# Performance work log

Measured on AMD Instinct MI355X. Metric: run time of the kernel, lower is better.

Reference implementation:

```python
import jax, jax.numpy as jnp
import numpy as np

N_NODES = 100000
N_EDGES = 1600000
IN_CH = 48
OUT_CH = 64
K = 2


def setup_inputs() -> dict:
    key = jax.random.key(0)
    k1, k2, k3, k4 = jax.random.split(key, 4)
    x = jax.random.normal(k1, (N_NODES, IN_CH), dtype=jnp.float32)
    edge_index = jax.random.randint(k2, (2, N_EDGES), 0, N_NODES, dtype=jnp.int64)
    W = jax.random.normal(k3, (IN_CH, OUT_CH), dtype=jnp.float32) * (1.0 / np.sqrt(IN_CH))
    b = jax.random.normal(k4, (OUT_CH,), dtype=jnp.float32) * 0.01
    return {"x": x, "edge_index": edge_index, "W": W, "b": b}


def _propagate(x, row, col):
    n = x.shape[0]
    # degree of each node counted over col (destination) indices
    deg = jax.ops.segment_sum(jnp.ones_like(col, dtype=x.dtype), col, num_segments=n)
    deg_inv_sqrt = jnp.where(deg > 0, jax.lax.rsqrt(jnp.where(deg > 0, deg, 1.0)), 0.0)
    norm = deg_inv_sqrt[row] * deg_inv_sqrt[col]  # [E]
    # gather-scale-scatter: out[col] += x[row] * norm
    msgs = x[row] * norm[:, None]  # [E, d]
    return jax.ops.segment_sum(msgs, col, num_segments=n)


def reference(x, edge_index, W, b):
    row, col = edge_index[0], edge_index[1]
    h = x
    for _ in range(K):
        h = _propagate(h, row, col)
    return h @ W + b
```

## Files before the change

kernel.cpp:

```cpp
#include <hip/hip_runtime.h>
#include <hip/hip_bf16.h>
#include <hip/hip_fp16.h>


#define N_NODES 100000
#define N_EDGES 1600000
#define IN_CH 48
#define OUT_CH 64
#define NBUCKETS 392
#define CAP 4608
#define EPB 8192
#define NBLK_EDGE 196
#define NBLK_BKT 391

__global__ void init_kernel(int* __restrict__ bucketCursor, int* __restrict__ binTotal) {
    int t = threadIdx.x;
    if (t < NBUCKETS) bucketCursor[t] = t * CAP;
    if (t < 64) binTotal[t] = 0;
}

__global__ void bucket_scatter_kernel(const int* __restrict__ row, const int* __restrict__ col,
                                      int* __restrict__ bucketCursor, int* __restrict__ edge_packed) {
    __shared__ int lh[NBUCKETS];
    __shared__ int lofs[NBUCKETS];
    __shared__ int lbase[NBUCKETS];
    __shared__ int stage[EPB];
    __shared__ unsigned short sbkt[EPB];
    __shared__ int wsum[4];
    int tid = threadIdx.x;
    int base = blockIdx.x * EPB;
    for (int i = tid; i < NBUCKETS; i += 256) lh[i] = 0;
    __syncthreads();
    #pragma unroll 4
    for (int k = 0; k < 32; k++) {
        int e = base + k * 256 + tid;
        if (e < N_EDGES) atomicAdd(&lh[col[e] >> 8], 1);
    }
    __syncthreads();
    {
        int c0 = (tid < 196) ? lh[2 * tid] : 0;
        int c1 = (tid < 196) ? lh[2 * tid + 1] : 0;
        int s = c0 + c1;
        int incl = s;
        int lane = tid & 63, w = tid >> 6;
        #pragma unroll
        for (int o = 1; o < 64; o <<= 1) {
            int v = __shfl_up(incl, o, 64);
            if (lane >= o) incl += v;
        }
        if (lane == 63) wsum[w] = incl;
        __syncthreads();
        int wbase = 0;
        for (int k = 0; k < w; k++) wbase += wsum[k];
        int ex = wbase + incl - s;
        if (tid < 196) {
            lofs[2 * tid]     = ex;
            lofs[2 * tid + 1] = ex + c0;
        }
    }
    __syncthreads();
    for (int i = tid; i < NBUCKETS; i += 256) {
        int c = lh[i];
        if (c > 0) lbase[i] = atomicAdd(&bucketCursor[i], c);
        lh[i] = 0;
    }
    __syncthreads();
    #pragma unroll 4
    for (int k = 0; k < 32; k++) {
        int e = base + k * 256 + tid;
        if (e < N_EDGES) {
            int c = col[e];
            int bkt = c >> 8;
            int r = atomicAdd(&lh[bkt], 1);
            int slot = lofs[bkt] + r;
            stage[slot] = (row[e] << 8) | (c & 255);
            sbkt[slot] = (unsigned short)bkt;
        }
    }
    __syncthreads();
    int total = (base + EPB <= N_EDGES) ? EPB : (N_EDGES - base);
    for (int i = tid; i < total; i += 256) {
        int bkt = sbkt[i];
        int dst = lbase[bkt] + (i - lofs[bkt]);
        if (dst < (bkt + 1) * CAP)
            edge_packed[dst] = stage[i];
    }
}

__global__ void fine_sort_kernel(const int* __restrict__ edge_packed,
                                 const int* __restrict__ bucketCursor,
                                 const float* __restrict__ x,
                                 int* __restrict__ edge_src,
                                 int* __restrict__ deg, int* __restrict__ start,
                                 float* __restrict__ dis, int* __restrict__ binTotal,
                                 __half2* __restrict__ xs) {
    __shared__ int fh[256];
    __shared__ int cur[256];
    __shared__ int bh[64];
    __shared__ float fdis[256];
    __shared__ int wsum2[4];
    int b = blockIdx.x;
    int t = threadIdx.x;
    int s0 = b * CAP;
    int s1 = min(bucketCursor[b], (b + 1) * CAP);
    int nodeBase = b << 8;
    fh[t] = 0;
    if (t < 64) bh[t] = 0;
    __syncthreads();
    for (int j = s0 + t; j < s1; j += 256)
        atomicAdd(&fh[edge_packed[j] & 255], 1);
    __syncthreads();
    int c = fh[t];
    int incl = c;
    {
        int sl = t & 63, sw = t >> 6;
        #pragma unroll
        for (int o = 1; o < 64; o <<= 1) {
            int v = __shfl_up(incl, o, 64);
            if (sl >= o) incl += v;
        }
        if (sl == 63) wsum2[sw] = incl;
        __syncthreads();
        int wbase = 0;
        for (int k = 0; k < sw; k++) wbase += wsum2[k];
        incl += wbase;
    }
    int ex = incl - c;
    int node = nodeBase + t;
    bool valid = (node < N_NODES);
    int d = c;
    float dv = (valid && d > 0) ? rsqrtf((float)d) : 0.0f;
    cur[t] = ex;
    fdis[t] = dv;
    if (valid) {
        deg[node] = d;
        start[node] = s0 + ex;
        dis[node] = dv;
        atomicAdd(&bh[min(d, 63)], 1);
    }
    __syncthreads();
    for (int i = t; i < 256 * 24; i += 256) {
        int ln = i / 24;
        int nd = nodeBase + ln;
        if (nd < N_NODES) {
            int ci = i - ln * 24;
            float dd = fdis[ln];
            float2 v = ((const float2*)x)[nd * 24 + ci];
            xs[nd * 24 + ci] = __floats2half2_rn(v.x * dd, v.y * dd);
        }
    }
    for (int j = s0 + t; j < s1; j += 256) {
        int rc = edge_packed[j];
        int p = atomicAdd(&cur[rc & 255], 1);
        edge_src[s0 + p] = rc >> 8;
    }
    __syncthreads();
    if (t < 64 && bh[t]) atomicAdd(&binTotal[t], bh[t]);
}

__global__ void binscan_kernel(const int* __restrict__ binTotal, int* __restrict__ binCursor) {
    if (threadIdx.x == 0) {
        int s = 0;
        for (int k = 63; k >= 0; k--) { binCursor[k] = s; s += binTotal[k]; }
    }
}

__global__ void order_kernel(const int* __restrict__ deg, const int* __restrict__ start,
                             const float* __restrict__ dis, int* __restrict__ binCursor,
                             int4* __restrict__ nodeinfo, int n) {
    __shared__ int lhist[64];
    __shared__ int lbase[64];
    int i = blockIdx.x * 256 + threadIdx.x;
    if (threadIdx.x < 64) lhist[threadIdx.x] = 0;
    __syncthreads();
    int bin = 0, myrank = 0;
    if (i < n) {
        bin = min(deg[i], 63);
        myrank = atomicAdd(&lhist[bin], 1);
    }
    __syncthreads();
    if (threadIdx.x < 64 && lhist[threadIdx.x] > 0)
        lbase[threadIdx.x] = atomicAdd(&binCursor[threadIdx.x], lhist[threadIdx.x]);
    __syncthreads();
    if (i < n)
        nodeinfo[lbase[bin] + myrank] = make_int4(i, start[i], deg[i], __float_as_int(dis[i]));
}

#define LOAD3(p, v0, v1, v2) { v0 = (p)[0]; v1 = (p)[1]; v2 = (p)[2]; }
#define ACC6(v0, v1, v2) { \
    float2 u0 = __half22float2(v0), u1 = __half22float2(v1), u2 = __half22float2(v2); \
    a0 += u0.x; a1 += u0.y; a2 += u1.x; a3 += u1.y; a4 += u2.x; a5 += u2.y; }
#define ACC6B(v0, v1, v2) { \
    float2 u0 = __half22float2(v0), u1 = __half22float2(v1), u2 = __half22float2(v2); \
    b0 += u0.x; b1 += u0.y; b2 += u1.x; b3 += u1.y; b4 += u2.x; b5 += u2.y; }

#define DECLD(P) __half2 P##00,P##01,P##02,P##10,P##11,P##12,P##20,P##21,P##22,P##30,P##31,P##32
#define DECLS(S) int S##0, S##1, S##2, S##3
#define LOADSRC(S) { S##0 = edge_src[j]; S##1 = edge_src[j+1]; \
                     S##2 = edge_src[j+2]; S##3 = edge_src[j+3]; j += 4; }
#define ISSUED(P, S, basep) { \
    const __half2* q0 = basep + S##0 * 24 + lane3; \
    const __half2* q1 = basep + S##1 * 24 + lane3; \
    const __half2* q2 = basep + S##2 * 24 + lane3; \
    const __half2* q3 = basep + S##3 * 24 + lane3; \
    P##00 = q0[0]; P##01 = q0[1]; P##02 = q0[2]; \
    P##10 = q1[0]; P##11 = q1[1]; P##12 = q1[2]; \
    P##20 = q2[0]; P##21 = q2[1]; P##22 = q2[2]; \
    P##30 = q3[0]; P##31 = q3[1]; P##32 = q3[2]; }
#define CONSUMED(P) { ACC6(P##00,P##01,P##02); ACC6B(P##10,P##11,P##12); \
                      ACC6(P##20,P##21,P##22); ACC6B(P##30,P##31,P##32); }

#define GATHER_PIPELINE(basep) { \
    int m = (e - s) >> 2; \
    DECLD(A); DECLD(B); \
    DECLS(sa); DECLS(sb); \
    if (m >= 2) { \
        LOADSRC(sa); LOADSRC(sb); \
        ISSUED(A, sa, basep); \
        m -= 2; \
        while (m >= 2) { \
            LOADSRC(sa); \
            ISSUED(B, sb, basep); \
            CONSUMED(A); \
            LOADSRC(sb); \
            ISSUED(A, sa, basep); \
            CONSUMED(B); \
            m -= 2; \
        } \
        if (m == 1) { \
            LOADSRC(sa); \
            ISSUED(B, sb, basep); \
            CONSUMED(A); \
            ISSUED(A, sa, basep); \
            CONSUMED(B); \
            CONSUMED(A); \
        } else { \
            ISSUED(B, sb, basep); \
            CONSUMED(A); \
            CONSUMED(B); \
        } \
    } else if (m == 1) { \
        LOADSRC(sa); \
        ISSUED(A, sa, basep); \
        CONSUMED(A); \
    } \
    for (; j < e; ++j) { \
        const __half2* p0 = basep + edge_src[j] * 24 + lane3; \
        __half2 v00, v01, v02; \
        LOAD3(p0, v00, v01, v02); \
        ACC6(v00, v01, v02); \
    } \
    a0 += b0; a1 += b1; a2 += b2; a3 += b3; a4 += b4; a5 += b5; }

__global__ void gather1_kernel(const __half2* __restrict__ xs,
                               const int* __restrict__ edge_src,
                               const int4* __restrict__ nodeinfo,
                               __half2* __restrict__ h1) {
    int g = blockIdx.x * 32 + (threadIdx.x >> 3);
    int lane3 = (threadIdx.x & 7) * 3;
    int4 ni = nodeinfo[g];
    int node = ni.x, s = ni.y, e = s + ni.z;
    float dv = __int_as_float(ni.w);
    float a0 = 0, a1 = 0, a2 = 0, a3 = 0, a4 = 0, a5 = 0;
    float b0 = 0, b1 = 0, b2 = 0, b3 = 0, b4 = 0, b5 = 0;
    int j = s;
    GATHER_PIPELINE(xs);
    float sc = dv * dv;
    __half2* q = h1 + node * 24 + lane3;
    q[0] = __floats2half2_rn(a0 * sc, a1 * sc);
    q[1] = __floats2half2_rn(a2 * sc, a3 * sc);
    q[2] = __floats2half2_rn(a4 * sc, a5 * sc);
}

__global__ void gather2_gemm_kernel(const __half2* __restrict__ h1,
                                    const int* __restrict__ edge_src,
                                    const int4* __restrict__ nodeinfo,
                                    const float* __restrict__ W,
                                    const float* __restrict__ bias,
                                    float* __restrict__ out) {
    __shared__ float sW[IN_CH * OUT_CH];
    __shared__ float sb[OUT_CH];
    __shared__ float sh[32][IN_CH + 1];

    for (int i = threadIdx.x; i < IN_CH * OUT_CH; i += 256) sW[i] = W[i];
    if (threadIdx.x < OUT_CH) sb[threadIdx.x] = bias[threadIdx.x];

    int nl = threadIdx.x >> 3;
    int lane = threadIdx.x & 7;
    int lane3 = lane * 3;
    int g = blockIdx.x * 32 + nl;
    int4 ni = nodeinfo[g];
    int node = ni.x, s = ni.y, e = s + ni.z;
    float dv = __int_as_float(ni.w);

    float a0 = 0, a1 = 0, a2 = 0, a3 = 0, a4 = 0, a5 = 0;
    float b0 = 0, b1 = 0, b2 = 0, b3 = 0, b4 = 0, b5 = 0;
    int j = s;
    GATHER_PIPELINE(h1);
    int c0 = 6 * lane;
    sh[nl][c0 + 0] = a0 * dv;
    sh[nl][c0 + 1] = a1 * dv;
    sh[nl][c0 + 2] = a2 * dv;
    sh[nl][c0 + 3] = a3 * dv;
    sh[nl][c0 + 4] = a4 * dv;
    sh[nl][c0 + 5] = a5 * dv;
    __syncthreads();

    int j0 = lane * 8;
    float acc[8];
    #pragma unroll
    for (int i = 0; i < 8; i++) acc[i] = sb[j0 + i];
    for (int k = 0; k < IN_CH; k++) {
        float s0 = sh[nl][k];
        #pragma unroll
        for (int i = 0; i < 8; i++) acc[i] += s0 * sW[k * OUT_CH + j0 + i];
    }
    float4* o = (float4*)(out + (size_t)node * OUT_CH + j0);
    o[0] = make_float4(acc[0], acc[1], acc[2], acc[3]);
    o[1] = make_float4(acc[4], acc[5], acc[6], acc[7]);
}

extern "C" void kernel_launch(void* const* d_in, const int* in_sizes, int n_in,
                              void* d_out, int out_size, void* d_ws, size_t ws_size,
                              hipStream_t stream) {
    const float* x   = (const float*)d_in[0];
    const int*   ei  = (const int*)d_in[1];
    const float* W   = (const float*)d_in[2];
    const float* b   = (const float*)d_in[3];
    float* out = (float*)d_out;

    const int* row = ei;
    const int* col = ei + N_EDGES;

    int* ws_i = (int*)d_ws;
    int* bucketCursor = ws_i;
    int* binTotal     = ws_i + 512;
    int* binCursor    = ws_i + 576;
    int* deg          = ws_i + 1024;
    int* start        = ws_i + 101376;
    float* dis        = (float*)(ws_i + 201728);
    int4* nodeinfo    = (int4*)(ws_i + 302080);
    int* edge_packed  = ws_i + 703488;
    int* edge_src     = ws_i + 2509824;
    __half2* xs       = (__half2*)(ws_i + 4316160);
    __half2* h1       = (__half2*)(ws_i + 6716160);

    init_kernel<<<1, 512, 0, stream>>>(bucketCursor, binTotal);
    bucket_scatter_kernel<<<NBLK_EDGE, 256, 0, stream>>>(row, col, bucketCursor, edge_packed);
    fine_sort_kernel<<<NBLK_BKT, 256, 0, stream>>>(edge_packed, bucketCursor, x,
                                                   edge_src, deg, start, dis, binTotal, xs);
    binscan_kernel<<<1, 64, 0, stream>>>(binTotal, binCursor);
    order_kernel<<<(N_NODES + 255) / 256, 256, 0, stream>>>(deg, start, dis, binCursor,
                                                            nodeinfo, N_NODES);

    gather1_kernel<<<N_NODES / 32, 256, 0, stream>>>(xs, edge_src, nodeinfo, h1);
    gather2_gemm_kernel<<<N_NODES / 32, 256, 0, stream>>>(h1, edge_src, nodeinfo, W, b, out);
}
```

Measured before the change: 228.2 us.

## Pad gather rows to 128B, split scaling kernel, shrink edge-bucketing blocks

Node feature rows in xs and h1 are padded from 24 to 32 half2, so each 96-byte row starts on a 128-byte boundary and gathers touch fewer cache lines. The x-scaling-to-fp16 work moves out of fine_sort into its own fully parallel scale_kernel, and xs reuses the edge_packed workspace region. The edge bucketing kernel now handles 2048 edges per block instead of 8192, giving more and lighter blocks. The trade-offs are a 33% larger feature footprint, one extra kernel launch, and more global atomics on the bucket cursors.

```diff
diff --git a/kernel.cpp b/kernel.cpp
--- a/kernel.cpp
+++ b/kernel.cpp
@@ -9,9 +9,11 @@
 #define OUT_CH 64
 #define NBUCKETS 392
 #define CAP 4608
-#define EPB 8192
-#define NBLK_EDGE 196
+#define EPB 2048
+#define EPR 8
+#define NBLK_EDGE 782
 #define NBLK_BKT 391
+#define RSTRIDE 32
 
 __global__ void init_kernel(int* __restrict__ bucketCursor, int* __restrict__ binTotal) {
     int t = threadIdx.x;
@@ -31,8 +33,8 @@
     int base = blockIdx.x * EPB;
     for (int i = tid; i < NBUCKETS; i += 256) lh[i] = 0;
     __syncthreads();
-    #pragma unroll 4
-    for (int k = 0; k < 32; k++) {
+    #pragma unroll
+    for (int k = 0; k < EPR; k++) {
         int e = base + k * 256 + tid;
         if (e < N_EDGES) atomicAdd(&lh[col[e] >> 8], 1);
     }
@@ -65,8 +67,8 @@
         lh[i] = 0;
     }
     __syncthreads();
-    #pragma unroll 4
-    for (int k = 0; k < 32; k++) {
+    #pragma unroll
+    for (int k = 0; k < EPR; k++) {
         int e = base + k * 256 + tid;
         if (e < N_EDGES) {
             int c = col[e];
@@ -89,15 +91,12 @@
 
 __global__ void fine_sort_kernel(const int* __restrict__ edge_packed,
                                  const int* __restrict__ bucketCursor,
-                                 const float* __restrict__ x,
                                  int* __restrict__ edge_src,
                                  int* __restrict__ deg, int* __restrict__ start,
-                                 float* __restrict__ dis, int* __restrict__ binTotal,
-                                 __half2* __restrict__ xs) {
+                                 float* __restrict__ dis, int* __restrict__ binTotal) {
     __shared__ int fh[256];
     __shared__ int cur[256];
     __shared__ int bh[64];
-    __shared__ float fdis[256];
     __shared__ int wsum2[4];
     int b = blockIdx.x;
     int t = threadIdx.x;
@@ -131,7 +130,6 @@
     int d = c;
     float dv = (valid && d > 0) ? rsqrtf((float)d) : 0.0f;
     cur[t] = ex;
-    fdis[t] = dv;
     if (valid) {
         deg[node] = d;
         start[node] = s0 + ex;
@@ -139,16 +137,6 @@
         atomicAdd(&bh[min(d, 63)], 1);
     }
     __syncthreads();
-    for (int i = t; i < 256 * 24; i += 256) {
-        int ln = i / 24;
-        int nd = nodeBase + ln;
-        if (nd < N_NODES) {
-            int ci = i - ln * 24;
-            float dd = fdis[ln];
-            float2 v = ((const float2*)x)[nd * 24 + ci];
-            xs[nd * 24 + ci] = __floats2half2_rn(v.x * dd, v.y * dd);
-        }
-    }
     for (int j = s0 + t; j < s1; j += 256) {
         int rc = edge_packed[j];
         int p = atomicAdd(&cur[rc & 255], 1);
@@ -156,6 +144,19 @@
     }
     __syncthreads();
     if (t < 64 && bh[t]) atomicAdd(&binTotal[t], bh[t]);
+}
+
+__global__ void scale_kernel(const float* __restrict__ x, const float* __restrict__ dis,
+                             __half2* __restrict__ xs) {
+    int g = blockIdx.x * 32 + (threadIdx.x >> 3);
+    int c = (threadIdx.x & 7) * 3;
+    float dd = dis[g];
+    const float2* px = (const float2*)x + g * 24 + c;
+    float2 v0 = px[0], v1 = px[1], v2 = px[2];
+    __half2* q = xs + g * RSTRIDE + c;
+    q[0] = __floats2half2_rn(v0.x * dd, v0.y * dd);
+    q[1] = __floats2half2_rn(v1.x * dd, v1.y * dd);
+    q[2] = __floats2half2_rn(v2.x * dd, v2.y * dd);
 }
 
 __global__ void binscan_kernel(const int* __restrict__ binTotal, int* __restrict__ binCursor) {
@@ -199,10 +200,10 @@
 #define LOADSRC(S) { S##0 = edge_src[j]; S##1 = edge_src[j+1]; \
                      S##2 = edge_src[j+2]; S##3 = edge_src[j+3]; j += 4; }
 #define ISSUED(P, S, basep) { \
-    const __half2* q0 = basep + S##0 * 24 + lane3; \
-    const __half2* q1 = basep + S##1 * 24 + lane3; \
-    const __half2* q2 = basep + S##2 * 24 + lane3; \
-    const __half2* q3 = basep + S##3 * 24 + lane3; \
+    const __half2* q0 = basep + S##0 * RSTRIDE + lane3; \
+    const __half2* q1 = basep + S##1 * RSTRIDE + lane3; \
+    const __half2* q2 = basep + S##2 * RSTRIDE + lane3; \
+    const __half2* q3 = basep + S##3 * RSTRIDE + lane3; \
     P##00 = q0[0]; P##01 = q0[1]; P##02 = q0[2]; \
     P##10 = q1[0]; P##11 = q1[1]; P##12 = q1[2]; \
     P##20 = q2[0]; P##21 = q2[1]; P##22 = q2[2]; \
@@ -245,7 +246,7 @@
         CONSUMED(A); \
     } \
     for (; j < e; ++j) { \
-        const __half2* p0 = basep + edge_src[j] * 24 + lane3; \
+        const __half2* p0 = basep + edge_src[j] * RSTRIDE + lane3; \
         __half2 v00, v01, v02; \
         LOAD3(p0, v00, v01, v02); \
         ACC6(v00, v01, v02); \
@@ -266,7 +267,7 @@
     int j = s;
     GATHER_PIPELINE(xs);
     float sc = dv * dv;
-    __half2* q = h1 + node * 24 + lane3;
+    __half2* q = h1 + node * RSTRIDE + lane3;
     q[0] = __floats2half2_rn(a0 * sc, a1 * sc);
     q[1] = __floats2half2_rn(a2 * sc, a3 * sc);
     q[2] = __floats2half2_rn(a4 * sc, a5 * sc);
@@ -341,14 +342,15 @@
     float* dis        = (float*)(ws_i + 201728);
     int4* nodeinfo    = (int4*)(ws_i + 302080);
     int* edge_packed  = ws_i + 703488;
-    int* edge_src     = ws_i + 2509824;
-    __half2* xs       = (__half2*)(ws_i + 4316160);
-    __half2* h1       = (__half2*)(ws_i + 6716160);
+    __half2* xs       = (__half2*)(ws_i + 703488);
+    int* edge_src     = ws_i + 3903488;
+    __half2* h1       = (__half2*)(ws_i + 5709824);
 
     init_kernel<<<1, 512, 0, stream>>>(bucketCursor, binTotal);
     bucket_scatter_kernel<<<NBLK_EDGE, 256, 0, stream>>>(row, col, bucketCursor, edge_packed);
-    fine_sort_kernel<<<NBLK_BKT, 256, 0, stream>>>(edge_packed, bucketCursor, x,
-                                                   edge_src, deg, start, dis, binTotal, xs);
+    fine_sort_kernel<<<NBLK_BKT, 256, 0, stream>>>(edge_packed, bucketCursor,
+                                                   edge_src, deg, start, dis, binTotal);
+    scale_kernel<<<N_NODES / 32, 256, 0, stream>>>(x, dis, xs);
     binscan_kernel<<<1, 64, 0, stream>>>(binTotal, binCursor);
     order_kernel<<<(N_NODES + 255) / 256, 256, 0, stream>>>(deg, start, dis, binCursor,
                                                             nodeinfo, N_NODES);
```

After: 211.2 us. 1.08x faster.
